# Kernel tuning notes

Hardware: AMD Instinct MI355X
Metric: run time of the kernel (lower is better)

## Reference

```python
import jax, jax.numpy as jnp
import numpy as np


def setup_inputs() -> dict:
    key = jax.random.key(0)
    ks = jax.random.split(key, 10)
    N, E, IN, H, OUT = 100000, 1250000, 64, 128, 64
    inp = {
        "x": jax.random.normal(ks[0], (N, IN), dtype=jnp.float32),
        "edge_index": jax.random.randint(ks[1], (2, E), 0, N, dtype=jnp.int64),
        "W1x": jax.random.normal(ks[2], (IN, H), dtype=jnp.float32) * 0.1,
        "b1x": jnp.zeros((H,), jnp.float32),
        "W2x": jax.random.normal(ks[3], (H, H), dtype=jnp.float32) * 0.1,
        "b2x": jnp.zeros((H,), jnp.float32),
        "W1a": jax.random.normal(ks[4], (IN, H), dtype=jnp.float32) * 0.1,
        "b1a": jnp.zeros((H,), jnp.float32),
        "W2a": jax.random.normal(ks[5], (H, H), dtype=jnp.float32) * 0.1,
        "b2a": jnp.zeros((H,), jnp.float32),
        "Wc": jax.random.normal(ks[6], (2 * H, H), dtype=jnp.float32) * 0.1,
        "bc": jnp.zeros((H,), jnp.float32),
        "Wcls": jax.random.normal(ks[7], (H, OUT), dtype=jnp.float32) * 0.1,
        "bcls": jnp.zeros((OUT,), jnp.float32),
        "num_nodes": N,
    }
    return inp


def _normalize_adj(edge_index, num_nodes):
    # add self loops, then D^{-1/2} A D^{-1/2} edge weights (deg counted on rows)
    loops = jnp.arange(num_nodes, dtype=edge_index.dtype)
    ei = jnp.concatenate([edge_index, jnp.stack([loops, loops])], axis=1)
    row, col = ei[0], ei[1]
    deg = jax.ops.segment_sum(jnp.ones(row.shape[0], jnp.float32), row,
                              num_segments=num_nodes)
    dinv = jnp.where(deg > 0, jax.lax.rsqrt(deg), 0.0)
    ew = dinv[row] * dinv[col]
    return row, col, ew


def reference(x, edge_index, W1x, b1x, W2x, b2x, W1a, b1a, W2a, b2a,
              Wc, bc, Wcls, bcls, num_nodes):
    row, col, ew = _normalize_adj(edge_index, num_nodes)
    # sparse adjacency aggregation: gather, scale, scatter-add
    agg = jax.ops.segment_sum(x[col] * ew[:, None], row, num_segments=num_nodes)
    # dual-branch MLPs
    h_x = jax.nn.relu(x @ W1x + b1x) @ W2x + b2x
    h_a = jax.nn.relu(agg @ W1a + b1a) @ W2a + b2a
    h = jnp.concatenate([h_x, h_a], axis=1) @ Wc + bc
    h = jax.nn.relu(h)  # dropout: eval mode (identity)
    return h @ Wcls + bcls
```

## Files before the change

### kernel.cpp

```cpp
#include <hip/hip_runtime.h>
#include <stdint.h>

typedef unsigned short u16;
typedef unsigned int u32;
typedef __attribute__((ext_vector_type(8))) short frag_ab;
typedef __attribute__((ext_vector_type(4))) float f32x4;

__device__ __forceinline__ u16 f2b(float f) {
  unsigned u = __float_as_uint(f);
  return (u16)((u + 0x7fffu + ((u >> 16) & 1u)) >> 16);
}
__device__ __forceinline__ float b2f(u16 u) {
  return __uint_as_float(((unsigned)u) << 16);
}

__device__ __forceinline__ int detect64(const int* __restrict__ ei32) {
  int v = ei32[2 * (threadIdx.x & 63) + 1];
  unsigned long long b = __ballot(v == 0);
  return (b == ~0ULL) ? 1 : 0;
}

__device__ __forceinline__ int edge_at(const void* ei, long pos, int is64) {
  if (is64) return (int)((const long long*)ei)[pos];
  return ((const int*)ei)[pos];
}

__global__ __launch_bounds__(256) void k_bhist_cvt(
    const void* __restrict__ ei, int E, int CH, int NB, int NBpad,
    int* __restrict__ bh,
    const float* __restrict__ x, u16* __restrict__ xb, long n64) {
  __shared__ int cnt[512];
  const int k = blockIdx.x, tid = threadIdx.x;
  const int is64 = detect64((const int*)ei);
  for (long i = ((long)k * 256 + tid) * 8; i < n64; i += 65536L * 8) {
    float4 v0 = *(const float4*)(x + i);
    float4 v1 = *(const float4*)(x + i + 4);
    frag_ab o;
    o[0] = (short)f2b(v0.x); o[1] = (short)f2b(v0.y);
    o[2] = (short)f2b(v0.z); o[3] = (short)f2b(v0.w);
    o[4] = (short)f2b(v1.x); o[5] = (short)f2b(v1.y);
    o[6] = (short)f2b(v1.z); o[7] = (short)f2b(v1.w);
    *(frag_ab*)(xb + i) = o;
  }
  for (int t = tid; t < NB; t += 256) cnt[t] = 0;
  __syncthreads();
  int e0 = k * CH, e1 = min(E, e0 + CH);
  for (int e = e0 + tid; e < e1; e += 256)
    atomicAdd(&cnt[edge_at(ei, e, is64) >> 9], 1);
  __syncthreads();
  for (int t = tid; t < NB; t += 256) bh[k * NBpad + t] = cnt[t];
}

__global__ __launch_bounds__(256) void k_cscan(
    int* __restrict__ bh, int* __restrict__ bstart, int NB, int NBpad, int E) {
  __shared__ int s[256];
  const int b = threadIdx.x;
  int tot = 0;
  if (b < NB)
    for (int k = 0; k < 256; ++k) tot += bh[k * NBpad + b];
  s[b] = (b < NB) ? tot : 0;
  __syncthreads();
  for (int off = 1; off < 256; off <<= 1) {
    int u = (b >= off) ? s[b - off] : 0;
    __syncthreads();
    s[b] += u;
    __syncthreads();
  }
  int excl = s[b] - tot;
  if (b < NB) {
    bstart[b] = excl;
    int run = excl;
    for (int k = 0; k < 256; ++k) {
      int t = bh[k * NBpad + b];
      bh[k * NBpad + b] = run;
      run += t;
    }
  }
  if (b == 0) bstart[NB] = E;
}

__global__ __launch_bounds__(256) void k_partition(
    const void* __restrict__ ei, int E, int CH, int NB, int NBpad,
    const int* __restrict__ bh, u32* __restrict__ staged) {
  __shared__ int cur[512];
  const int k = blockIdx.x, tid = threadIdx.x;
  const int is64 = detect64((const int*)ei);
  for (int t = tid; t < NB; t += 256) cur[t] = bh[k * NBpad + t];
  __syncthreads();
  int e0 = k * CH, e1 = min(E, e0 + CH);
  for (int e = e0 + tid; e < e1; e += 256) {
    int r = edge_at(ei, e, is64);
    int c = edge_at(ei, (long)E + e, is64);
    int pos = atomicAdd(&cur[r >> 9], 1);
    staged[pos] = ((u32)(r & 511) << 23) | (u32)c;
  }
}

__global__ __launch_bounds__(1024) void k_csr_bucket(
    const u32* __restrict__ staged, const int* __restrict__ bstart,
    int* __restrict__ rowptr, float* __restrict__ dinv,
    u32* __restrict__ cols, int N, int E) {
  __shared__ int cnt[512];
  __shared__ int cur[512];
  const int b = blockIdx.x, tid = threadIdx.x;
  const int r0 = b << 9;
  if (tid < 512) cnt[tid] = 0;
  __syncthreads();
  const int j0 = bstart[b], j1 = bstart[b + 1];
  for (int j = j0 + tid; j < j1; j += 1024)
    atomicAdd(&cnt[staged[j] >> 23], 1);
  __syncthreads();
  if (tid < 512) cur[tid] = cnt[tid];
  __syncthreads();
  for (int off = 1; off < 512; off <<= 1) {
    int v = 0;
    if (tid < 512 && tid >= off) v = cur[tid - off];
    __syncthreads();
    if (tid < 512) cur[tid] += v;
    __syncthreads();
  }
  int myStart = 0;
  if (tid < 512) {
    myStart = j0 + cur[tid] - cnt[tid];
    int r = r0 + tid;
    if (r < N) {
      rowptr[r] = myStart;
      dinv[r] = rsqrtf((float)cnt[tid] + 1.0f);
    }
  }
  __syncthreads();
  if (tid < 512) cur[tid] = myStart;
  if (b == 0 && tid == 0) rowptr[N] = E;
  __syncthreads();
  for (int j = j0 + tid; j < j1; j += 1024) {
    u32 v = staged[j];
    int rl = v >> 23;
    int pos = atomicAdd(&cur[rl], 1);
    cols[pos] = v & 0x7FFFFF;
  }
}

__global__ __launch_bounds__(256) void k_aggregate(
    const int* __restrict__ rowptr, const u32* __restrict__ cols,
    const u16* __restrict__ xb, const float* __restrict__ dinv,
    u16* __restrict__ aggb, int N) {
  int q = (blockIdx.x * 256 + threadIdx.x) >> 6;
  int f = threadIdx.x & 63;
  int r0 = q * 2, r1 = q * 2 + 1;
  if (r0 >= N) return;
  const bool has1 = (r1 < N);
  int j0 = rowptr[r0], e0 = rowptr[r0 + 1];
  int j1 = has1 ? rowptr[r1] : 0;
  int e1 = has1 ? rowptr[r1 + 1] : 0;
  float d0 = dinv[r0];
  float d1 = has1 ? dinv[r1] : 0.f;
  float acc0 = b2f(xb[(long)r0 * 64 + f]) * d0;
  float acc1 = has1 ? b2f(xb[(long)r1 * 64 + f]) * d1 : 0.f;
  while (j0 + 4 <= e0 && j1 + 4 <= e1) {
    int ca0 = cols[j0], ca1 = cols[j0 + 1], ca2 = cols[j0 + 2], ca3 = cols[j0 + 3];
    int cb0 = cols[j1], cb1 = cols[j1 + 1], cb2 = cols[j1 + 2], cb3 = cols[j1 + 3];
    float xa0 = b2f(xb[(long)ca0 * 64 + f]);
    float xa1 = b2f(xb[(long)ca1 * 64 + f]);
    float xa2 = b2f(xb[(long)ca2 * 64 + f]);
    float xa3 = b2f(xb[(long)ca3 * 64 + f]);
    float xb0 = b2f(xb[(long)cb0 * 64 + f]);
    float xb1 = b2f(xb[(long)cb1 * 64 + f]);
    float xb2 = b2f(xb[(long)cb2 * 64 + f]);
    float xb3 = b2f(xb[(long)cb3 * 64 + f]);
    float wa0 = dinv[ca0], wa1 = dinv[ca1], wa2 = dinv[ca2], wa3 = dinv[ca3];
    float wb0 = dinv[cb0], wb1 = dinv[cb1], wb2 = dinv[cb2], wb3 = dinv[cb3];
    acc0 = fmaf(xa0, wa0, acc0); acc1 = fmaf(xb0, wb0, acc1);
    acc0 = fmaf(xa1, wa1, acc0); acc1 = fmaf(xb1, wb1, acc1);
    acc0 = fmaf(xa2, wa2, acc0); acc1 = fmaf(xb2, wb2, acc1);
    acc0 = fmaf(xa3, wa3, acc0); acc1 = fmaf(xb3, wb3, acc1);
    j0 += 4; j1 += 4;
  }
  for (; j0 + 4 <= e0; j0 += 4) {
    int c0 = cols[j0], c1 = cols[j0 + 1], c2 = cols[j0 + 2], c3 = cols[j0 + 3];
    float x0 = b2f(xb[(long)c0 * 64 + f]);
    float x1 = b2f(xb[(long)c1 * 64 + f]);
    float x2 = b2f(xb[(long)c2 * 64 + f]);
    float x3 = b2f(xb[(long)c3 * 64 + f]);
    acc0 = fmaf(x0, dinv[c0], acc0);
    acc0 = fmaf(x1, dinv[c1], acc0);
    acc0 = fmaf(x2, dinv[c2], acc0);
    acc0 = fmaf(x3, dinv[c3], acc0);
  }
  for (; j0 < e0; ++j0) {
    int c = cols[j0];
    acc0 = fmaf(b2f(xb[(long)c * 64 + f]), dinv[c], acc0);
  }
  for (; j1 + 4 <= e1; j1 += 4) {
    int c0 = cols[j1], c1 = cols[j1 + 1], c2 = cols[j1 + 2], c3 = cols[j1 + 3];
    float x0 = b2f(xb[(long)c0 * 64 + f]);
    float x1 = b2f(xb[(long)c1 * 64 + f]);
    float x2 = b2f(xb[(long)c2 * 64 + f]);
    float x3 = b2f(xb[(long)c3 * 64 + f]);
    acc1 = fmaf(x0, dinv[c0], acc1);
    acc1 = fmaf(x1, dinv[c1], acc1);
    acc1 = fmaf(x2, dinv[c2], acc1);
    acc1 = fmaf(x3, dinv[c3], acc1);
  }
  for (; j1 < e1; ++j1) {
    int c = cols[j1];
    acc1 = fmaf(b2f(xb[(long)c * 64 + f]), dinv[c], acc1);
  }
  aggb[(long)r0 * 64 + f] = f2b(acc0 * d0);
  if (has1) aggb[(long)r1 * 64 + f] = f2b(acc1 * d1);
}

__global__ __launch_bounds__(256) void k_wpack(
    const float* __restrict__ W1x, const float* __restrict__ W1a,
    const float* __restrict__ W2x, const float* __restrict__ W2a,
    const float* __restrict__ Wc, const float* __restrict__ b2x,
    const float* __restrict__ b2a, const float* __restrict__ bc,
    const float* __restrict__ Wcls,
    u16* __restrict__ W1xf, u16* __restrict__ W1af,
    u16* __restrict__ Wxpf, u16* __restrict__ Wapf,
    u16* __restrict__ Wclsf, float* __restrict__ bp) {
  const int blk = blockIdx.x, t = threadIdx.x;
  if (blk < 128) {
    const bool isX = blk < 64;
    int i = (isX ? blk : blk - 64) * 256 + t;
    const float* W2 = isX ? W2x : W2a;
    const float* wc = isX ? Wc : Wc + 128 * 128;
    int b = i & 7, l = (i >> 3) & 63, fi = i >> 9;
    int kb = fi & 3, nb = fi >> 2;
    int k = kb * 32 + (l >> 4) * 8 + b;
    int n = nb * 16 + (l & 15);
    float s = 0.f;
    for (int m = 0; m < 128; ++m) s = fmaf(W2[k * 128 + m], wc[m * 128 + n], s);
    (isX ? Wxpf : Wapf)[i] = f2b(s);
  } else if (blk < 224) {
    const float* W; u16* dst; int K, Nc, i0;
    if (blk < 160)      { W = W1x;  dst = W1xf;  K = 64;  Nc = 128; i0 = blk - 128; }
    else if (blk < 192) { W = W1a;  dst = W1af;  K = 64;  Nc = 128; i0 = blk - 160; }
    else                { W = Wcls; dst = Wclsf; K = 128; Nc = 64;  i0 = blk - 192; }
    int i = i0 * 256 + t;
    if (i < K * Nc) {
      int b = i & 7, l = (i >> 3) & 63, fi = i >> 9;
      int KB = K >> 5;
      int kb = fi % KB, nb = fi / KB;
      int k = kb * 32 + (l >> 4) * 8 + b;
      int n = nb * 16 + (l & 15);
      dst[i] = f2b(W[k * Nc + n]);
    }
  } else if (t < 128) {
    float s = bc[t];
    for (int m = 0; m < 128; ++m)
      s += b2x[m] * Wc[m * 128 + t] + b2a[m] * Wc[(128 + m) * 128 + t];
    bp[t] = s;
  }
}

__global__ __launch_bounds__(256) void k_mlp(
    const u16* __restrict__ xb, const u16* __restrict__ aggb,
    const u16* __restrict__ W1xf, const u16* __restrict__ W1af,
    const float* __restrict__ b1x, const float* __restrict__ b1a,
    const u16* __restrict__ Wxpf, const u16* __restrict__ Wapf,
    const float* __restrict__ bp,
    const u16* __restrict__ Wclsf, const float* __restrict__ bcls,
    float* __restrict__ out, int N) {
  __shared__ u16 H1[4][16 * 256];
  __shared__ u16 H2[4][16 * 128];
  const int w = threadIdx.x >> 6;
  const int lane = threadIdx.x & 63;
  const int m0 = blockIdx.x * 64 + w * 16;
  const int lm = lane & 15;
  const int lq = lane >> 4;
  u16* h1 = H1[w];
  u16* h2 = H2[w];

  for (int br = 0; br < 2; ++br) {
    const u16* A = br ? aggb : xb;
    const u16* Wf = br ? W1af : W1xf;
    const float* bias = br ? b1a : b1x;
    const u16* ap = A + (long)(m0 + lm) * 64 + lq * 8;
    frag_ab a0 = *(const frag_ab*)(ap);
    frag_ab a1 = *(const frag_ab*)(ap + 32);
#pragma unroll
    for (int nb = 0; nb < 8; ++nb) {
      frag_ab b0 = *(const frag_ab*)(Wf + (size_t)((nb * 2 + 0) * 64 + lane) * 8);
      frag_ab b1v = *(const frag_ab*)(Wf + (size_t)((nb * 2 + 1) * 64 + lane) * 8);
      f32x4 acc = {0.f, 0.f, 0.f, 0.f};
      acc = __builtin_amdgcn_mfma_f32_16x16x32_bf16(a0, b0, acc, 0, 0, 0);
      acc = __builtin_amdgcn_mfma_f32_16x16x32_bf16(a1, b1v, acc, 0, 0, 0);
      int col = nb * 16 + lm;
      float bv = bias[col];
#pragma unroll
      for (int r = 0; r < 4; ++r) {
        int row = lq * 4 + r;
        h1[(row * 256 + br * 128 + col) ^ ((row & 7) << 3)] =
            f2b(fmaxf(acc[r] + bv, 0.f));
      }
    }
  }
  __syncthreads();

  frag_ab hfr[8];
#pragma unroll
  for (int kb = 0; kb < 8; ++kb)
    hfr[kb] = *(const frag_ab*)&h1[(lm * 256 + kb * 32 + lq * 8) ^ ((lm & 7) << 3)];
#pragma unroll
  for (int nb = 0; nb < 8; ++nb) {
    f32x4 acc = {0.f, 0.f, 0.f, 0.f};
#pragma unroll
    for (int kb = 0; kb < 8; ++kb) {
      const u16* Wf2 = (kb < 4) ? Wxpf : Wapf;
      frag_ab b = *(const frag_ab*)(Wf2 + (size_t)((nb * 4 + (kb & 3)) * 64 + lane) * 8);
      acc = __builtin_amdgcn_mfma_f32_16x16x32_bf16(hfr[kb], b, acc, 0, 0, 0);
    }
    int col = nb * 16 + lm;
    float bv = bp[col];
#pragma unroll
    for (int r = 0; r < 4; ++r) {
      int row = lq * 4 + r;
      h2[(row * 128 + col) ^ ((row & 7) << 3)] = f2b(fmaxf(acc[r] + bv, 0.f));
    }
  }
  __syncthreads();

  frag_ab h3[4];
#pragma unroll
  for (int kb = 0; kb < 4; ++kb)
    h3[kb] = *(const frag_ab*)&h2[(lm * 128 + kb * 32 + lq * 8) ^ ((lm & 7) << 3)];
#pragma unroll
  for (int nb = 0; nb < 4; ++nb) {
    f32x4 acc = {0.f, 0.f, 0.f, 0.f};
#pragma unroll
    for (int kb = 0; kb < 4; ++kb) {
      frag_ab b = *(const frag_ab*)(Wclsf + (size_t)((nb * 4 + kb) * 64 + lane) * 8);
      acc = __builtin_amdgcn_mfma_f32_16x16x32_bf16(h3[kb], b, acc, 0, 0, 0);
    }
    int col = nb * 16 + lm;
    float bv = bcls[col];
#pragma unroll
    for (int r = 0; r < 4; ++r) {
      int grow = m0 + lq * 4 + r;
      if (grow < N) out[(long)grow * 64 + col] = acc[r] + bv;
    }
  }
}

extern "C" void kernel_launch(void* const* d_in, const int* in_sizes, int n_in,
                              void* d_out, int out_size, void* d_ws, size_t ws_size,
                              hipStream_t stream) {
  const float* x    = (const float*)d_in[0];
  const void*  ei   = d_in[1];
  const float* W1x  = (const float*)d_in[2];
  const float* b1x  = (const float*)d_in[3];
  const float* W2x  = (const float*)d_in[4];
  const float* b2x  = (const float*)d_in[5];
  const float* W1a  = (const float*)d_in[6];
  const float* b1a  = (const float*)d_in[7];
  const float* W2a  = (const float*)d_in[8];
  const float* b2a  = (const float*)d_in[9];
  const float* Wc   = (const float*)d_in[10];
  const float* bc   = (const float*)d_in[11];
  const float* Wcls = (const float*)d_in[12];
  const float* bcls = (const float*)d_in[13];
  const int N = in_sizes[0] / 64;
  const int E = in_sizes[1] / 2;

  const int NB = (N + 511) >> 9;
  const int NBpad = (NB + 63) & ~63;
  const int CH = (E + 255) / 256;

  float* ws = (float*)d_ws;
  long nAlign = (N + 255) & ~255L;
  float* dinv = ws;
  int*   rowptr = (int*)(ws + nAlign);
  u16*   xb   = (u16*)(ws + 2 * nAlign + 256);
  u16*   aggb = xb + (long)N * 64;
  float* bp   = (float*)(aggb + (long)N * 64);
  u16*   W1xf = (u16*)(bp + 128);
  u16*   W1af = W1xf + 8192;
  u16*   Wxpf = W1af + 8192;
  u16*   Wapf = Wxpf + 16384;
  u16*   Wclsf = Wapf + 16384;
  int*   bh   = (int*)(Wclsf + 8192);
  int*   bstart = bh + 256 * NBpad;
  u32*   staged = (u32*)(bstart + NB + 64);
  u32*   cols   = staged + E;
  float* out = (float*)d_out;

  k_bhist_cvt<<<256, 256, 0, stream>>>(ei, E, CH, NB, NBpad, bh, x, xb, (long)N * 64);
  k_cscan<<<1, 256, 0, stream>>>(bh, bstart, NB, NBpad, E);
  k_partition<<<256, 256, 0, stream>>>(ei, E, CH, NB, NBpad, bh, staged);
  k_csr_bucket<<<NB, 1024, 0, stream>>>(staged, bstart, rowptr, dinv, cols, N, E);
  k_aggregate<<<(N + 7) / 8, 256, 0, stream>>>(rowptr, cols, xb, dinv, aggb, N);
  k_wpack<<<225, 256, 0, stream>>>(W1x, W1a, W2x, W2a, Wc, b2x, b2a, bc, Wcls,
                                   W1xf, W1af, Wxpf, Wapf, Wclsf, bp);
  k_mlp<<<(N + 63) / 64, 256, 0, stream>>>(xb, aggb, W1xf, W1af, b1x, b1a,
                                           Wxpf, Wapf, bp, Wclsf, bcls, out, N);
}
```

Baseline: 157.7 us.

## Split MLP kernel work across warps by output columns instead of rows

The fused MLP kernel now has each of the four warps compute a slice of output columns for all 64 rows of the block, rather than every column for its own 16 rows. Each warp therefore loads only its share of the weight fragments from global memory, cutting per-block weight traffic about fourfold. The hidden activations now live in one shared tile that all warps read, so the intermediate layers are read back from LDS per row tile instead of held in registers. In exchange this adds LDS read traffic and block-wide synchronisation, and the first layer still loads all 64 input rows in every warp.

```diff
diff --git a/kernel.cpp b/kernel.cpp
--- a/kernel.cpp
+++ b/kernel.cpp
@@ -261,84 +261,99 @@
     const float* __restrict__ bp,
     const u16* __restrict__ Wclsf, const float* __restrict__ bcls,
     float* __restrict__ out, int N) {
-  __shared__ u16 H1[4][16 * 256];
-  __shared__ u16 H2[4][16 * 128];
+  __shared__ u16 H1[64 * 256];
+  __shared__ u16 H2[64 * 128];
   const int w = threadIdx.x >> 6;
   const int lane = threadIdx.x & 63;
-  const int m0 = blockIdx.x * 64 + w * 16;
+  const int m0 = blockIdx.x * 64;
   const int lm = lane & 15;
   const int lq = lane >> 4;
-  u16* h1 = H1[w];
-  u16* h2 = H2[w];
 
   for (int br = 0; br < 2; ++br) {
     const u16* A = br ? aggb : xb;
     const u16* Wf = br ? W1af : W1xf;
     const float* bias = br ? b1a : b1x;
-    const u16* ap = A + (long)(m0 + lm) * 64 + lq * 8;
-    frag_ab a0 = *(const frag_ab*)(ap);
-    frag_ab a1 = *(const frag_ab*)(ap + 32);
-#pragma unroll
-    for (int nb = 0; nb < 8; ++nb) {
+    frag_ab a[4][2];
+#pragma unroll
+    for (int rt = 0; rt < 4; ++rt) {
+      const u16* ap = A + (long)(m0 + rt * 16 + lm) * 64 + lq * 8;
+      a[rt][0] = *(const frag_ab*)(ap);
+      a[rt][1] = *(const frag_ab*)(ap + 32);
+    }
+#pragma unroll
+    for (int nbl = 0; nbl < 2; ++nbl) {
+      int nb = w * 2 + nbl;
       frag_ab b0 = *(const frag_ab*)(Wf + (size_t)((nb * 2 + 0) * 64 + lane) * 8);
-      frag_ab b1v = *(const frag_ab*)(Wf + (size_t)((nb * 2 + 1) * 64 + lane) * 8);
-      f32x4 acc = {0.f, 0.f, 0.f, 0.f};
-      acc = __builtin_amdgcn_mfma_f32_16x16x32_bf16(a0, b0, acc, 0, 0, 0);
-      acc = __builtin_amdgcn_mfma_f32_16x16x32_bf16(a1, b1v, acc, 0, 0, 0);
+      frag_ab b1 = *(const frag_ab*)(Wf + (size_t)((nb * 2 + 1) * 64 + lane) * 8);
       int col = nb * 16 + lm;
       float bv = bias[col];
 #pragma unroll
-      for (int r = 0; r < 4; ++r) {
-        int row = lq * 4 + r;
-        h1[(row * 256 + br * 128 + col) ^ ((row & 7) << 3)] =
-            f2b(fmaxf(acc[r] + bv, 0.f));
+      for (int rt = 0; rt < 4; ++rt) {
+        f32x4 acc = {0.f, 0.f, 0.f, 0.f};
+        acc = __builtin_amdgcn_mfma_f32_16x16x32_bf16(a[rt][0], b0, acc, 0, 0, 0);
+        acc = __builtin_amdgcn_mfma_f32_16x16x32_bf16(a[rt][1], b1, acc, 0, 0, 0);
+#pragma unroll
+        for (int r = 0; r < 4; ++r) {
+          int row = rt * 16 + lq * 4 + r;
+          H1[(row * 256 + br * 128 + col) ^ ((row & 7) << 3)] =
+              f2b(fmaxf(acc[r] + bv, 0.f));
+        }
       }
     }
   }
   __syncthreads();
 
-  frag_ab hfr[8];
-#pragma unroll
-  for (int kb = 0; kb < 8; ++kb)
-    hfr[kb] = *(const frag_ab*)&h1[(lm * 256 + kb * 32 + lq * 8) ^ ((lm & 7) << 3)];
-#pragma unroll
-  for (int nb = 0; nb < 8; ++nb) {
-    f32x4 acc = {0.f, 0.f, 0.f, 0.f};
+#pragma unroll
+  for (int nbl = 0; nbl < 2; ++nbl) {
+    int nb = w * 2 + nbl;
+    f32x4 acc[4] = {{0.f,0.f,0.f,0.f},{0.f,0.f,0.f,0.f},
+                    {0.f,0.f,0.f,0.f},{0.f,0.f,0.f,0.f}};
 #pragma unroll
     for (int kb = 0; kb < 8; ++kb) {
       const u16* Wf2 = (kb < 4) ? Wxpf : Wapf;
       frag_ab b = *(const frag_ab*)(Wf2 + (size_t)((nb * 4 + (kb & 3)) * 64 + lane) * 8);
-      acc = __builtin_amdgcn_mfma_f32_16x16x32_bf16(hfr[kb], b, acc, 0, 0, 0);
+#pragma unroll
+      for (int rt = 0; rt < 4; ++rt) {
+        int row = rt * 16 + lm;
+        frag_ab a = *(const frag_ab*)&H1[(row * 256 + kb * 32 + lq * 8) ^ ((lm & 7) << 3)];
+        acc[rt] = __builtin_amdgcn_mfma_f32_16x16x32_bf16(a, b, acc[rt], 0, 0, 0);
+      }
     }
     int col = nb * 16 + lm;
     float bv = bp[col];
 #pragma unroll
-    for (int r = 0; r < 4; ++r) {
-      int row = lq * 4 + r;
-      h2[(row * 128 + col) ^ ((row & 7) << 3)] = f2b(fmaxf(acc[r] + bv, 0.f));
-    }
-  }
-  __syncthreads();
-
-  frag_ab h3[4];
-#pragma unroll
-  for (int kb = 0; kb < 4; ++kb)
-    h3[kb] = *(const frag_ab*)&h2[(lm * 128 + kb * 32 + lq * 8) ^ ((lm & 7) << 3)];
-#pragma unroll
-  for (int nb = 0; nb < 4; ++nb) {
-    f32x4 acc = {0.f, 0.f, 0.f, 0.f};
+    for (int rt = 0; rt < 4; ++rt)
+#pragma unroll
+      for (int r = 0; r < 4; ++r) {
+        int row = rt * 16 + lq * 4 + r;
+        H2[(row * 128 + col) ^ ((row & 7) << 3)] = f2b(fmaxf(acc[rt][r] + bv, 0.f));
+      }
+  }
+  __syncthreads();
+
+  {
+    const int nb = w;
+    f32x4 acc[4] = {{0.f,0.f,0.f,0.f},{0.f,0.f,0.f,0.f},
+                    {0.f,0.f,0.f,0.f},{0.f,0.f,0.f,0.f}};
 #pragma unroll
     for (int kb = 0; kb < 4; ++kb) {
       frag_ab b = *(const frag_ab*)(Wclsf + (size_t)((nb * 4 + kb) * 64 + lane) * 8);
-      acc = __builtin_amdgcn_mfma_f32_16x16x32_bf16(h3[kb], b, acc, 0, 0, 0);
+#pragma unroll
+      for (int rt = 0; rt < 4; ++rt) {
+        int row = rt * 16 + lm;
+        frag_ab a = *(const frag_ab*)&H2[(row * 128 + kb * 32 + lq * 8) ^ ((lm & 7) << 3)];
+        acc[rt] = __builtin_amdgcn_mfma_f32_16x16x32_bf16(a, b, acc[rt], 0, 0, 0);
+      }
     }
     int col = nb * 16 + lm;
     float bv = bcls[col];
 #pragma unroll
-    for (int r = 0; r < 4; ++r) {
-      int grow = m0 + lq * 4 + r;
-      if (grow < N) out[(long)grow * 64 + col] = acc[r] + bv;
-    }
+    for (int rt = 0; rt < 4; ++rt)
+#pragma unroll
+      for (int r = 0; r < 4; ++r) {
+        int grow = m0 + rt * 16 + lq * 4 + r;
+        if (grow < N) out[(long)grow * 64 + col] = acc[rt][r] + bv;
+      }
   }
 }
 
```

Result: no change. 159.5 us (+1.1%).
